# Kernel tuning notes

Measured on AMD Instinct MI355X. Metric: run time of the kernel, lower is better.

## Reference

```python
import jax, jax.numpy as jnp
import numpy as np

B = 16
C = 80
LEVELS = [(128, 128, 8), (64, 64, 16), (32, 32, 32), (16, 16, 64), (8, 8, 128)]
TOPN = 1000
MIN_SCORE = 0.05
NMS_THR = 0.6
MAX_OBJ = 100


def setup_inputs() -> dict:
    key = jax.random.key(0)
    inp = {}
    for l, (H, W, s) in enumerate(LEVELS):
        key, k1, k2, k3 = jax.random.split(key, 4)
        inp[f"cls{l}"] = jax.random.uniform(k1, (B, H, W, C), jnp.float32)
        inp[f"reg{l}"] = jax.random.uniform(k2, (B, H, W, 4), jnp.float32) * 128.0
        inp[f"ctr{l}"] = jax.random.uniform(k3, (B, H, W, 1), jnp.float32)
        xs = (jnp.arange(W, dtype=jnp.float32) + 0.5) * s
        ys = (jnp.arange(H, dtype=jnp.float32) + 0.5) * s
        gx, gy = jnp.meshgrid(xs, ys)  # [H, W]
        pos = jnp.stack([gx, gy], axis=-1)  # [H, W, 2]
        inp[f"pos{l}"] = jnp.broadcast_to(pos, (B, H, W, 2))
    return inp


def _nms_one(scores, classes, bboxes):
    # scores [N], classes int32 [N], bboxes float [N, 4] (already int-truncated values)
    s = jnp.where(scores > MIN_SCORE, scores, -jnp.inf)  # score-threshold mask
    top_s, top_i = jax.lax.top_k(s, TOPN)  # sort descending, keep topn
    top_c = jax.lax.stop_gradient(classes[top_i].astype(jnp.float32))
    top_b = bboxes[top_i]
    valid = top_s > MIN_SCORE
    wh = top_b[:, 2:4] - top_b[:, 0:2]
    areas = jnp.clip(wh[:, 0] * wh[:, 1], 0.0001)
    ar = jnp.arange(TOPN)

    def body(i, suppressed):
        active = valid[i] & (~suppressed[i])
        b = top_b[i]
        tl = jnp.maximum(b[0:2], top_b[:, 0:2])
        br = jnp.minimum(b[2:4], top_b[:, 2:4])
        owh = jnp.clip(br - tl, 0.0)
        inter = owh[:, 0] * owh[:, 1]
        union = jnp.clip(areas[i] + areas - inter, 0.0001)
        iou = inter / union
        return suppressed | (active & (ar > i) & (iou >= NMS_THR))

    suppressed = jax.lax.fori_loop(0, TOPN, body, jnp.zeros((TOPN,), bool))
    keep = valid & (~suppressed)
    rank = jnp.cumsum(keep.astype(jnp.int32)) - 1
    # scatter kept detections (in score order) into first MAX_OBJ slots; slot MAX_OBJ is a dump
    idx = jnp.where(keep & (rank < MAX_OBJ), rank, MAX_OBJ)
    out_s = jnp.full((MAX_OBJ + 1,), -1.0, jnp.float32).at[idx].set(jnp.where(keep, top_s, -1.0))[:MAX_OBJ]
    out_c = jnp.full((MAX_OBJ + 1,), -1.0, jnp.float32).at[idx].set(jnp.where(keep, top_c, -1.0))[:MAX_OBJ]
    out_b = jnp.zeros((MAX_OBJ + 1, 4), jnp.float32).at[idx].set(jnp.where(keep[:, None], top_b, 0.0))[:MAX_OBJ]
    return out_s, out_c, out_b


def _forward(cls_list, reg_list, ctr_list, pos_list):
    ss, cc, bb = [], [], []
    for c, r, t, p in zip(cls_list, reg_list, ctr_list, pos_list):
        b = c.shape[0]
        c = c.reshape(b, -1, c.shape[-1])   # [B, HW, 80]
        r = r.reshape(b, -1, 4)             # [B, HW, 4]
        t = t.reshape(b, -1)                # [B, HW]
        p = p.reshape(b, -1, 2)             # [B, HW, 2]
        sc = jnp.sqrt(jnp.max(c, axis=2) * t)
        cl = jnp.argmax(c, axis=2).astype(jnp.int32)
        bmin = p - r[:, :, 0:2]
        bmax = p + r[:, :, 2:4]
        # torch .int() truncates toward zero; values are used as floats afterward
        box = jax.lax.stop_gradient(jnp.trunc(jnp.concatenate([bmin, bmax], axis=2)))
        ss.append(sc); cc.append(cl); bb.append(box)
    scores = jnp.concatenate(ss, axis=1)
    classes = jnp.concatenate(cc, axis=1)
    boxes = jnp.concatenate(bb, axis=1)
    return jax.vmap(_nms_one)(scores, classes, boxes)


def reference(cls0, cls1, cls2, cls3, cls4, reg0, reg1, reg2, reg3, reg4,
              ctr0, ctr1, ctr2, ctr3, ctr4, pos0, pos1, pos2, pos3, pos4):
    return _forward([cls0, cls1, cls2, cls3, cls4],
                    [reg0, reg1, reg2, reg3, reg4],
                    [ctr0, ctr1, ctr2, ctr3, ctr4],
                    [pos0, pos1, pos2, pos3, pos4])
```

## Files before the change

kernel.cpp:

```cpp
#include <hip/hip_runtime.h>
#include <stdint.h>

typedef unsigned int u32;
typedef unsigned long long u64;

#define NTOT 21824
#define NBATCH 16
#define TOPN 1000
#define MAXOBJ 100
#define CAPC 8192
#define BINBASE 15616
#define NBINS 1024

__device__ __forceinline__ void locate(
    int b, int loc,
    const float* __restrict__ cls0, const float* __restrict__ cls1,
    const float* __restrict__ cls2, const float* __restrict__ cls3,
    const float* __restrict__ cls4,
    const float* __restrict__ ctr0, const float* __restrict__ ctr1,
    const float* __restrict__ ctr2, const float* __restrict__ ctr3,
    const float* __restrict__ ctr4,
    const float*& cp, const float*& tp)
{
    if (loc < 16384)      { size_t o = (size_t)b*16384 + loc;          cp = cls0 + o*80; tp = ctr0 + o; }
    else if (loc < 20480) { size_t o = (size_t)b*4096  + (loc-16384);  cp = cls1 + o*80; tp = ctr1 + o; }
    else if (loc < 21504) { size_t o = (size_t)b*1024  + (loc-20480);  cp = cls2 + o*80; tp = ctr2 + o; }
    else if (loc < 21760) { size_t o = (size_t)b*256   + (loc-21504);  cp = cls3 + o*80; tp = ctr3 + o; }
    else                  { size_t o = (size_t)b*64    + (loc-21760);  cp = cls4 + o*80; tp = ctr4 + o; }
}

__global__ __launch_bounds__(256) void decode_kernel(
    const float* __restrict__ cls0, const float* __restrict__ cls1,
    const float* __restrict__ cls2, const float* __restrict__ cls3,
    const float* __restrict__ cls4,
    const float* __restrict__ ctr0, const float* __restrict__ ctr1,
    const float* __restrict__ ctr2, const float* __restrict__ ctr3,
    const float* __restrict__ ctr4,
    u32* __restrict__ keys, int* __restrict__ clsidx)
{
    int tid = threadIdx.x;
    int g = tid >> 2, j = tid & 3;
    int b = blockIdx.y;
    int loc0 = blockIdx.x * 128 + g;
    int loc1 = loc0 + 64;
    bool v1 = (loc1 < NTOT);

    const float *cp0, *tp0, *cp1, *tp1;
    locate(b, loc0, cls0, cls1, cls2, cls3, cls4, ctr0, ctr1, ctr2, ctr3, ctr4, cp0, tp0);
    locate(b, v1 ? loc1 : loc0, cls0, cls1, cls2, cls3, cls4, ctr0, ctr1, ctr2, ctr3, ctr4, cp1, tp1);

    const float4* c40 = (const float4*)cp0;
    const float4* c41 = (const float4*)cp1;
    float4 a0[5], a1[5];
#pragma unroll
    for (int q = 0; q < 5; ++q) a0[q] = c40[j + 4*q];
#pragma unroll
    for (int q = 0; q < 5; ++q) a1[q] = c41[j + 4*q];
    float t0v = *tp0;
    float t1v = *tp1;

    float maxv0 = -1.0f; int arg0 = 0;
    float maxv1 = -1.0f; int arg1 = 0;
#pragma unroll
    for (int q = 0; q < 5; ++q) {
        float4 v = a0[q];
        int ch = 16*q + 4*j;
        if (v.x > maxv0) { maxv0 = v.x; arg0 = ch;     }
        if (v.y > maxv0) { maxv0 = v.y; arg0 = ch + 1; }
        if (v.z > maxv0) { maxv0 = v.z; arg0 = ch + 2; }
        if (v.w > maxv0) { maxv0 = v.w; arg0 = ch + 3; }
    }
#pragma unroll
    for (int q = 0; q < 5; ++q) {
        float4 v = a1[q];
        int ch = 16*q + 4*j;
        if (v.x > maxv1) { maxv1 = v.x; arg1 = ch;     }
        if (v.y > maxv1) { maxv1 = v.y; arg1 = ch + 1; }
        if (v.z > maxv1) { maxv1 = v.z; arg1 = ch + 2; }
        if (v.w > maxv1) { maxv1 = v.w; arg1 = ch + 3; }
    }
#pragma unroll
    for (int d = 1; d <= 2; d <<= 1) {
        float ov = __shfl_xor(maxv0, d);
        int   oa = __shfl_xor(arg0, d);
        if (ov > maxv0 || (ov == maxv0 && oa < arg0)) { maxv0 = ov; arg0 = oa; }
        float ow = __shfl_xor(maxv1, d);
        int   ob = __shfl_xor(arg1, d);
        if (ow > maxv1 || (ow == maxv1 && ob < arg1)) { maxv1 = ow; arg1 = ob; }
    }
    if (j == 0) {
        float score0 = sqrtf(maxv0 * t0v);
        u32 key0 = (score0 > 0.05f) ? (__float_as_uint(score0) | 0x80000000u) : 0u;
        size_t o0 = (size_t)b * NTOT + loc0;
        keys[o0] = key0;
        clsidx[o0] = arg0;
        if (v1) {
            float score1 = sqrtf(maxv1 * t1v);
            u32 key1 = (score1 > 0.05f) ? (__float_as_uint(score1) | 0x80000000u) : 0u;
            size_t o1 = (size_t)b * NTOT + loc1;
            keys[o1] = key1;
            clsidx[o1] = arg1;
        }
    }
}

__global__ __launch_bounds__(1024) void pivot_kernel(
    const u32* __restrict__ keys, u32* __restrict__ params, u32* __restrict__ gcnt,
    float* __restrict__ tscore, float* __restrict__ tcls, float4* __restrict__ tbox)
{
    __shared__ u32 shist[NBINS];
    __shared__ u32 s_wtot[16];
    __shared__ int s_tf;
    int b = blockIdx.x, tid = threadIdx.x;
    int lane = tid & 63, wave = tid >> 6;
    const u32* kb = keys + (size_t)b * NTOT;

    for (int i = tid; i < TOPN; i += 1024) {
        size_t o = (size_t)b * TOPN + i;
        tscore[o] = -1.0f; tcls[o] = -1.0f;
        tbox[o] = make_float4(0.f, 0.f, 0.f, 0.f);
    }
    shist[tid] = 0;
    if (tid == 0) { s_tf = -1; gcnt[b * 32] = 0; }
    __syncthreads();

    for (int i = tid; i < NTOT; i += 1024) {
        u32 k = kb[i];
        if (k) {
            int v = (int)((k >> 16) & 0x7FFFu) - BINBASE;
            v = v < 0 ? 0 : (v > NBINS - 1 ? NBINS - 1 : v);
            atomicAdd(&shist[v], 1u);
        }
    }
    __syncthreads();

    u32 h = shist[tid];
    u32 x = h;
#pragma unroll
    for (int off = 1; off < 64; off <<= 1) {
        u32 y = __shfl_down(x, off);
        if (lane + off < 64) x += y;
    }
    if (lane == 0) s_wtot[wave] = x;
    __syncthreads();
    u32 wsuf = 0, tot = 0;
    for (int w2 = 0; w2 < 16; ++w2) { u32 v = s_wtot[w2]; tot += v; if (w2 > wave) wsuf += v; }
    u32 suffix_incl = x + wsuf;
    u32 target = (tot < TOPN) ? tot : TOPN;

    if (target > 0 && suffix_incl >= target) atomicMax(&s_tf, tid);
    __syncthreads();
    if (tid == 0) {
        int t0 = s_tf;
        u32 P;
        if (target == 0)        P = 0xFFFFFFFFu;
        else if (tot <= TOPN)   P = 1u;
        else                    P = ((u32)(t0 + BINBASE) << 16) | 0x80000000u;
        params[2 * b] = P;
        params[2 * b + 1] = target;
    }
}

__global__ __launch_bounds__(256) void gather_kernel(
    const u32* __restrict__ keys, const u32* __restrict__ params,
    u64* __restrict__ candbuf, u32* __restrict__ gcnt)
{
    __shared__ u32 s_wcnt[4];
    __shared__ u32 s_base;
    int b = blockIdx.y;
    int tid = threadIdx.x;
    int lane = tid & 63, wave = tid >> 6;
    u32 P = params[2 * b];
    int i = blockIdx.x * 256 + tid;
    u32 k = (i < NTOT) ? keys[(size_t)b * NTOT + i] : 0u;
    bool pass = (k != 0u) && (k >= P);
    u64 mask = __ballot(pass);
    if (lane == 0) s_wcnt[wave] = (u32)__popcll(mask);
    __syncthreads();
    if (tid == 0) {
        u32 tot = s_wcnt[0] + s_wcnt[1] + s_wcnt[2] + s_wcnt[3];
        s_base = tot ? atomicAdd(&gcnt[b * 32], tot) : 0u;
    }
    __syncthreads();
    if (pass) {
        u32 woff = 0;
        for (int w2 = 0; w2 < wave; ++w2) woff += s_wcnt[w2];
        u32 pos = s_base + woff + (u32)__popcll(mask & ((1ull << lane) - 1ull));
        if (pos < CAPC)
            candbuf[(size_t)b * CAPC + pos] = ((u64)k << 32) | (u32)(~i);
    }
}

__global__ __launch_bounds__(256) void rank_kernel(
    const u64* __restrict__ candbuf, const u32* __restrict__ gcnt,
    const u32* __restrict__ params,
    const int* __restrict__ clsidx,
    const float* __restrict__ reg0, const float* __restrict__ reg1,
    const float* __restrict__ reg2, const float* __restrict__ reg3,
    const float* __restrict__ reg4,
    float* __restrict__ tscore, float* __restrict__ tcls, float4* __restrict__ tbox)
{
    int b = blockIdx.y;
    int lane = threadIdx.x & 63;
    u32 M = gcnt[b * 32]; if (M > CAPC) M = CAPC;
    u32 target = params[2 * b + 1];
    const u64* cb = candbuf + (size_t)b * CAPC;
    u32 Mr = (M + 63u) & ~63u;

    u32 wbase0 = blockIdx.x * 256 + (threadIdx.x & ~63u);
    for (u32 base = wbase0; base < M; base += 8 * 256) {
        u32 i0 = base + lane;
        bool val = (i0 < M);
        u64 e = val ? cb[i0] : ~0ull;
        u32 r = 0;
        for (u32 c0 = 0; c0 < Mr; c0 += 64) {
            u32 j = c0 + lane;
            u64 v = (j < M) ? cb[j] : 0ull;
            u32 vlo = (u32)v, vhi = (u32)(v >> 32);
#pragma unroll
            for (int s = 0; s < 64; ++s) {
                u32 lo = (u32)__builtin_amdgcn_readlane((int)vlo, s);
                u32 hi = (u32)__builtin_amdgcn_readlane((int)vhi, s);
                u64 vj = ((u64)hi << 32) | lo;
                r += (vj > e) ? 1u : 0u;
            }
        }
        if (val && r < target) {
            u32 k = (u32)(e >> 32);
            u32 loc = ~(u32)e;
            const float* rp; float st; u32 li; int wsh;
            if (loc < 16384u)      { li = loc;          wsh = 7; st = 8.f;   rp = reg0 + ((size_t)b*16384 + li)*4; }
            else if (loc < 20480u) { li = loc - 16384u; wsh = 6; st = 16.f;  rp = reg1 + ((size_t)b*4096  + li)*4; }
            else if (loc < 21504u) { li = loc - 20480u; wsh = 5; st = 32.f;  rp = reg2 + ((size_t)b*1024  + li)*4; }
            else if (loc < 21760u) { li = loc - 21504u; wsh = 4; st = 64.f;  rp = reg3 + ((size_t)b*256   + li)*4; }
            else                   { li = loc - 21760u; wsh = 3; st = 128.f; rp = reg4 + ((size_t)b*64    + li)*4; }
            u32 wx = li & ((1u << wsh) - 1u);
            u32 hy = li >> wsh;
            float px = ((float)wx + 0.5f) * st;
            float py = ((float)hy + 0.5f) * st;
            float4 rg = *(const float4*)rp;
            float4 bx;
            bx.x = truncf(px - rg.x); bx.y = truncf(py - rg.y);
            bx.z = truncf(px + rg.z); bx.w = truncf(py + rg.w);
            size_t src = (size_t)b * NTOT + loc;
            size_t o = (size_t)b * TOPN + r;
            tscore[o] = __uint_as_float(k & 0x7FFFFFFFu);
            tcls[o] = (float)clsidx[src];
            tbox[o] = bx;
        }
    }
}

__global__ __launch_bounds__(256) void iou_kernel(
    const float4* __restrict__ tbox, u64* __restrict__ sup)
{
    __shared__ float4 sbox[TOPN];
    int b = blockIdx.y;
    int tid = threadIdx.x, lane = tid & 63, wave = tid >> 6;
    const float4* tb = tbox + (size_t)b * TOPN;
    for (int i = tid; i < TOPN; i += 256) sbox[i] = tb[i];
    __syncthreads();
    int i = blockIdx.x * 4 + wave;
    float4 bi = sbox[i];
    float areai = fmaxf((bi.z - bi.x) * (bi.w - bi.y), 0.0001f);
    u64* row = sup + ((size_t)b * TOPN + i) * 16;
#pragma unroll
    for (int w = 0; w < 16; ++w) {
        int col = w * 64 + lane;
        bool bit = false;
        if (col < TOPN) {
            float4 bj = sbox[col];
            float areaj = fmaxf((bj.z - bj.x) * (bj.w - bj.y), 0.0001f);
            float tlx = fmaxf(bi.x, bj.x), tly = fmaxf(bi.y, bj.y);
            float brx = fminf(bi.z, bj.z), bry = fminf(bi.w, bj.w);
            float ow = fmaxf(brx - tlx, 0.f), oh = fmaxf(bry - tly, 0.f);
            float inter = ow * oh;
            float uni = fmaxf(areai + areaj - inter, 0.0001f);
            bit = (col > i) && (inter / uni >= 0.6f);
        }
        u64 m = __ballot(bit);
        if (lane == 0) row[w] = m;
    }
}

#define CHROWS 128
#define NCHUNK 8

__global__ __launch_bounds__(1024) void finalize_kernel(
    const float* __restrict__ tscore, const float* __restrict__ tcls,
    const float4* __restrict__ tbox, const u64* __restrict__ sup,
    float* __restrict__ out)
{
    __shared__ u64 mat[2][CHROWS * 16];
    __shared__ u32 validsh[TOPN];
    __shared__ u64 removed_sh[16];
    __shared__ u32 wpref[17];
    int b = blockIdx.x, tid = threadIdx.x;
    int wave = tid >> 6, lane = tid & 63;

    for (int i = tid; i < TOPN; i += 1024)
        validsh[i] = (tscore[(size_t)b * TOPN + i] > 0.05f) ? 1u : 0u;

    const u64* supb = sup + (size_t)b * TOPN * 16;
    for (int idx = tid; idx < CHROWS * 16; idx += 1024)
        mat[0][idx] = supb[idx];
    __syncthreads();

    u64 my = 0;
    if (wave == 0) {
#pragma unroll
        for (int w2 = 0; w2 < 16; ++w2) {
            int i = w2 * 64 + lane;
            bool v = (i < TOPN) ? (validsh[i] != 0) : false;
            u64 m = __ballot(v);
            if (lane == w2) my = ~m;
        }
    }

    for (int chunk = 0; chunk < NCHUNK; ++chunk) {
        if (wave > 0 && chunk + 1 < NCHUNK) {
            int nr = (chunk + 1 == NCHUNK - 1) ? (TOPN - (NCHUNK - 1) * CHROWS) : CHROWS;
            const u64* src = supb + (size_t)(chunk + 1) * CHROWS * 16;
            u64* dst = mat[(chunk + 1) & 1];
            for (int idx = tid - 64; idx < nr * 16; idx += 960)
                dst[idx] = src[idx];
        }
        if (wave == 0) {
            int r0 = chunk * CHROWS;
            int rows = (chunk == NCHUNK - 1) ? (TOPN - r0) : CHROWS;
            int lw = lane & 15;
            const u64* M = mat[chunk & 1];
            for (int sub = 0; sub < rows; sub += 64) {
                int w2 = (r0 + sub) >> 6;
                u64 cur = __shfl(my, w2);
                int nsub = rows - sub; if (nsub > 64) nsub = 64;
                const u64* R = M + sub * 16;
                int ngrp = nsub >> 3;
                u64 cme[8], cww[8];
#pragma unroll
                for (int g = 0; g < 8; ++g) { cme[g] = R[g*16 + lw]; cww[g] = R[g*16 + w2]; }
                for (int grp = 0; grp < ngrp; ++grp) {
                    u64 nme[8] = {0,0,0,0,0,0,0,0}, nww[8] = {0,0,0,0,0,0,0,0};
                    if (grp + 1 < ngrp) {
                        const u64* Rn = R + (grp + 1) * 128;
#pragma unroll
                        for (int g = 0; g < 8; ++g) { nme[g] = Rn[g*16 + lw]; nww[g] = Rn[g*16 + w2]; }
                    }
#pragma unroll
                    for (int g = 0; g < 8; ++g) {
                        int u = grp * 8 + g;
                        u64 bit = (cur >> u) & 1ull;
                        u64 act = bit - 1ull;
                        cur |= cww[g] & act;
                        my  |= cme[g] & act;
                    }
#pragma unroll
                    for (int g = 0; g < 8; ++g) { cme[g] = nme[g]; cww[g] = nww[g]; }
                }
            }
        }
        __syncthreads();
    }
    if (wave == 0) {
        if (lane < 16) removed_sh[lane] = my;
        u32 pc = (lane < 16) ? (u32)__popcll(~my) : 0u;
#pragma unroll
        for (int off = 1; off < 16; off <<= 1) {
            u32 y = __shfl_up(pc, off);
            if (lane >= off) pc += y;
        }
        if (lane < 16) wpref[lane + 1] = pc;
        if (lane == 0) wpref[0] = 0;
    }
    __syncthreads();

    float* out_s = out;
    float* out_c = out + NBATCH * MAXOBJ;
    float* out_b = out + 2 * NBATCH * MAXOBJ;
    if (tid < MAXOBJ)     { out_s[b * MAXOBJ + tid] = -1.f; out_c[b * MAXOBJ + tid] = -1.f; }
    if (tid < MAXOBJ * 4) out_b[b * MAXOBJ * 4 + tid] = 0.f;
    __syncthreads();
    if (tid < TOPN) {
        u64 kw = ~removed_sh[tid >> 6];
        if ((kw >> (tid & 63)) & 1ull) {
            int rank = (int)wpref[tid >> 6] + (int)__popcll(kw & ((1ull << (tid & 63)) - 1ull));
            if (rank < MAXOBJ) {
                size_t o = (size_t)b * TOPN + tid;
                out_s[b * MAXOBJ + rank] = tscore[o];
                out_c[b * MAXOBJ + rank] = tcls[o];
                ((float4*)out_b)[b * MAXOBJ + rank] = tbox[o];
            }
        }
    }
}

extern "C" void kernel_launch(void* const* d_in, const int* in_sizes, int n_in,
                              void* d_out, int out_size, void* d_ws, size_t ws_size,
                              hipStream_t stream) {
    (void)in_sizes; (void)n_in; (void)out_size; (void)ws_size;
    const float* cls[5]; const float* reg[5]; const float* ctr[5];
    for (int l = 0; l < 5; ++l) {
        cls[l] = (const float*)d_in[4 * l + 0];
        reg[l] = (const float*)d_in[4 * l + 1];
        ctr[l] = (const float*)d_in[4 * l + 2];
    }
    char* w = (char*)d_ws;
    u32*    keys   = (u32*)(w + 0);
    int*    clsidx = (int*)(w + 1396736);
    float*  tscore = (float*)(w + 2793472);
    float*  tcls   = (float*)(w + 2857472);
    float4* tbox   = (float4*)(w + 2921472);
    u64*    sup    = (u64*)(w + 3177472);
    u64*    candbuf= (u64*)(w + 3177472);
    u32*    gcnt   = (u32*)(w + 5225472);
    u32*    params = (u32*)(w + 5227520);

    decode_kernel<<<dim3((NTOT + 127) / 128, NBATCH), 256, 0, stream>>>(
        cls[0], cls[1], cls[2], cls[3], cls[4],
        ctr[0], ctr[1], ctr[2], ctr[3], ctr[4],
        keys, clsidx);
    pivot_kernel<<<NBATCH, 1024, 0, stream>>>(keys, params, gcnt, tscore, tcls, tbox);
    gather_kernel<<<dim3((NTOT + 255) / 256, NBATCH), 256, 0, stream>>>(keys, params, candbuf, gcnt);
    rank_kernel<<<dim3(8, NBATCH), 256, 0, stream>>>(candbuf, gcnt, params, clsidx,
                                                     reg[0], reg[1], reg[2], reg[3], reg[4],
                                                     tscore, tcls, tbox);
    iou_kernel<<<dim3(TOPN / 4, NBATCH), 256, 0, stream>>>(tbox, sup);
    finalize_kernel<<<NBATCH, 1024, 0, stream>>>(tscore, tcls, tbox, sup, (float*)d_out);
}
```

Baseline: 269.6 us.

## Fuse pivot, gather and rank into one per-batch top-k kernel with LDS candidates

Merges the histogram-pivot, candidate-gather and rank kernels into a single 1024-thread block per batch image. Candidates are compacted into shared memory instead of a global buffer, and the rank pass reads them from LDS. This removes two launches and the global round trips for params, counters and candidates. The cost is that the O(M²) ranking now runs on only 16 blocks instead of 128, which cuts parallelism, and 64KB of LDS is used per block. Decode also handles four locations per thread instead of two.

```diff
diff --git a/kernel.cpp b/kernel.cpp
--- a/kernel.cpp
+++ b/kernel.cpp
@@ -8,7 +8,7 @@
 #define NBATCH 16
 #define TOPN 1000
 #define MAXOBJ 100
-#define CAPC 8192
+#define LCAP 8192
 #define BINBASE 15616
 #define NBINS 1024
 
@@ -41,76 +41,77 @@
     int tid = threadIdx.x;
     int g = tid >> 2, j = tid & 3;
     int b = blockIdx.y;
-    int loc0 = blockIdx.x * 128 + g;
-    int loc1 = loc0 + 64;
-    bool v1 = (loc1 < NTOT);
-
-    const float *cp0, *tp0, *cp1, *tp1;
-    locate(b, loc0, cls0, cls1, cls2, cls3, cls4, ctr0, ctr1, ctr2, ctr3, ctr4, cp0, tp0);
-    locate(b, v1 ? loc1 : loc0, cls0, cls1, cls2, cls3, cls4, ctr0, ctr1, ctr2, ctr3, ctr4, cp1, tp1);
-
-    const float4* c40 = (const float4*)cp0;
-    const float4* c41 = (const float4*)cp1;
-    float4 a0[5], a1[5];
-#pragma unroll
-    for (int q = 0; q < 5; ++q) a0[q] = c40[j + 4*q];
-#pragma unroll
-    for (int q = 0; q < 5; ++q) a1[q] = c41[j + 4*q];
-    float t0v = *tp0;
-    float t1v = *tp1;
-
-    float maxv0 = -1.0f; int arg0 = 0;
-    float maxv1 = -1.0f; int arg1 = 0;
-#pragma unroll
-    for (int q = 0; q < 5; ++q) {
-        float4 v = a0[q];
-        int ch = 16*q + 4*j;
-        if (v.x > maxv0) { maxv0 = v.x; arg0 = ch;     }
-        if (v.y > maxv0) { maxv0 = v.y; arg0 = ch + 1; }
-        if (v.z > maxv0) { maxv0 = v.z; arg0 = ch + 2; }
-        if (v.w > maxv0) { maxv0 = v.w; arg0 = ch + 3; }
-    }
-#pragma unroll
-    for (int q = 0; q < 5; ++q) {
-        float4 v = a1[q];
-        int ch = 16*q + 4*j;
-        if (v.x > maxv1) { maxv1 = v.x; arg1 = ch;     }
-        if (v.y > maxv1) { maxv1 = v.y; arg1 = ch + 1; }
-        if (v.z > maxv1) { maxv1 = v.z; arg1 = ch + 2; }
-        if (v.w > maxv1) { maxv1 = v.w; arg1 = ch + 3; }
+    int base = blockIdx.x * 256;
+
+    const float* cp[4]; const float* tp[4]; bool v[4];
+#pragma unroll
+    for (int c = 0; c < 4; ++c) {
+        v[c] = (base + 64 * c) < NTOT;
+        int loc = v[c] ? (base + 64 * c + g) : (base + g);
+        locate(b, loc, cls0, cls1, cls2, cls3, cls4,
+               ctr0, ctr1, ctr2, ctr3, ctr4, cp[c], tp[c]);
+    }
+
+    float4 a[4][5];
+#pragma unroll
+    for (int c = 0; c < 4; ++c) {
+        const float4* c4 = (const float4*)cp[c];
+#pragma unroll
+        for (int q = 0; q < 5; ++q) a[c][q] = c4[j + 4*q];
+    }
+    float tv[4];
+#pragma unroll
+    for (int c = 0; c < 4; ++c) tv[c] = *tp[c];
+
+    float maxv[4]; int arg[4];
+#pragma unroll
+    for (int c = 0; c < 4; ++c) {
+        maxv[c] = -1.0f; arg[c] = 0;
+#pragma unroll
+        for (int q = 0; q < 5; ++q) {
+            float4 vv = a[c][q];
+            int ch = 16*q + 4*j;
+            if (vv.x > maxv[c]) { maxv[c] = vv.x; arg[c] = ch;     }
+            if (vv.y > maxv[c]) { maxv[c] = vv.y; arg[c] = ch + 1; }
+            if (vv.z > maxv[c]) { maxv[c] = vv.z; arg[c] = ch + 2; }
+            if (vv.w > maxv[c]) { maxv[c] = vv.w; arg[c] = ch + 3; }
+        }
     }
 #pragma unroll
     for (int d = 1; d <= 2; d <<= 1) {
-        float ov = __shfl_xor(maxv0, d);
-        int   oa = __shfl_xor(arg0, d);
-        if (ov > maxv0 || (ov == maxv0 && oa < arg0)) { maxv0 = ov; arg0 = oa; }
-        float ow = __shfl_xor(maxv1, d);
-        int   ob = __shfl_xor(arg1, d);
-        if (ow > maxv1 || (ow == maxv1 && ob < arg1)) { maxv1 = ow; arg1 = ob; }
+#pragma unroll
+        for (int c = 0; c < 4; ++c) {
+            float ov = __shfl_xor(maxv[c], d);
+            int   oa = __shfl_xor(arg[c], d);
+            if (ov > maxv[c] || (ov == maxv[c] && oa < arg[c])) { maxv[c] = ov; arg[c] = oa; }
+        }
     }
     if (j == 0) {
-        float score0 = sqrtf(maxv0 * t0v);
-        u32 key0 = (score0 > 0.05f) ? (__float_as_uint(score0) | 0x80000000u) : 0u;
-        size_t o0 = (size_t)b * NTOT + loc0;
-        keys[o0] = key0;
-        clsidx[o0] = arg0;
-        if (v1) {
-            float score1 = sqrtf(maxv1 * t1v);
-            u32 key1 = (score1 > 0.05f) ? (__float_as_uint(score1) | 0x80000000u) : 0u;
-            size_t o1 = (size_t)b * NTOT + loc1;
-            keys[o1] = key1;
-            clsidx[o1] = arg1;
-        }
-    }
-}
-
-__global__ __launch_bounds__(1024) void pivot_kernel(
-    const u32* __restrict__ keys, u32* __restrict__ params, u32* __restrict__ gcnt,
+#pragma unroll
+        for (int c = 0; c < 4; ++c) {
+            if (v[c]) {
+                float score = sqrtf(maxv[c] * tv[c]);
+                u32 key = (score > 0.05f) ? (__float_as_uint(score) | 0x80000000u) : 0u;
+                size_t o = (size_t)b * NTOT + base + 64 * c + g;
+                keys[o] = key;
+                clsidx[o] = arg[c];
+            }
+        }
+    }
+}
+
+__global__ __launch_bounds__(1024) void topk_kernel(
+    const u32* __restrict__ keys, const int* __restrict__ clsidx,
+    const float* __restrict__ reg0, const float* __restrict__ reg1,
+    const float* __restrict__ reg2, const float* __restrict__ reg3,
+    const float* __restrict__ reg4,
     float* __restrict__ tscore, float* __restrict__ tcls, float4* __restrict__ tbox)
 {
+    __shared__ u64 cand[LCAP];
     __shared__ u32 shist[NBINS];
     __shared__ u32 s_wtot[16];
     __shared__ int s_tf;
+    __shared__ u32 s_cnt;
     int b = blockIdx.x, tid = threadIdx.x;
     int lane = tid & 63, wave = tid >> 6;
     const u32* kb = keys + (size_t)b * NTOT;
@@ -121,7 +122,7 @@
         tbox[o] = make_float4(0.f, 0.f, 0.f, 0.f);
     }
     shist[tid] = 0;
-    if (tid == 0) { s_tf = -1; gcnt[b * 32] = 0; }
+    if (tid == 0) { s_tf = -1; s_cnt = 0; }
     __syncthreads();
 
     for (int i = tid; i < NTOT; i += 1024) {
@@ -150,73 +151,40 @@
 
     if (target > 0 && suffix_incl >= target) atomicMax(&s_tf, tid);
     __syncthreads();
-    if (tid == 0) {
+    u32 P;
+    {
         int t0 = s_tf;
-        u32 P;
         if (target == 0)        P = 0xFFFFFFFFu;
         else if (tot <= TOPN)   P = 1u;
         else                    P = ((u32)(t0 + BINBASE) << 16) | 0x80000000u;
-        params[2 * b] = P;
-        params[2 * b + 1] = target;
-    }
-}
-
-__global__ __launch_bounds__(256) void gather_kernel(
-    const u32* __restrict__ keys, const u32* __restrict__ params,
-    u64* __restrict__ candbuf, u32* __restrict__ gcnt)
-{
-    __shared__ u32 s_wcnt[4];
-    __shared__ u32 s_base;
-    int b = blockIdx.y;
-    int tid = threadIdx.x;
-    int lane = tid & 63, wave = tid >> 6;
-    u32 P = params[2 * b];
-    int i = blockIdx.x * 256 + tid;
-    u32 k = (i < NTOT) ? keys[(size_t)b * NTOT + i] : 0u;
-    bool pass = (k != 0u) && (k >= P);
-    u64 mask = __ballot(pass);
-    if (lane == 0) s_wcnt[wave] = (u32)__popcll(mask);
-    __syncthreads();
-    if (tid == 0) {
-        u32 tot = s_wcnt[0] + s_wcnt[1] + s_wcnt[2] + s_wcnt[3];
-        s_base = tot ? atomicAdd(&gcnt[b * 32], tot) : 0u;
-    }
-    __syncthreads();
-    if (pass) {
-        u32 woff = 0;
-        for (int w2 = 0; w2 < wave; ++w2) woff += s_wcnt[w2];
-        u32 pos = s_base + woff + (u32)__popcll(mask & ((1ull << lane) - 1ull));
-        if (pos < CAPC)
-            candbuf[(size_t)b * CAPC + pos] = ((u64)k << 32) | (u32)(~i);
-    }
-}
-
-__global__ __launch_bounds__(256) void rank_kernel(
-    const u64* __restrict__ candbuf, const u32* __restrict__ gcnt,
-    const u32* __restrict__ params,
-    const int* __restrict__ clsidx,
-    const float* __restrict__ reg0, const float* __restrict__ reg1,
-    const float* __restrict__ reg2, const float* __restrict__ reg3,
-    const float* __restrict__ reg4,
-    float* __restrict__ tscore, float* __restrict__ tcls, float4* __restrict__ tbox)
-{
-    int b = blockIdx.y;
-    int lane = threadIdx.x & 63;
-    u32 M = gcnt[b * 32]; if (M > CAPC) M = CAPC;
-    u32 target = params[2 * b + 1];
-    const u64* cb = candbuf + (size_t)b * CAPC;
+    }
+
+    for (int base = 0; base < NTOT; base += 1024) {
+        int i = base + tid;
+        u32 k = (i < NTOT) ? kb[i] : 0u;
+        bool pass = (k != 0u) && (k >= P);
+        u64 mask = __ballot(pass);
+        u32 wbase = 0;
+        if (lane == 0 && mask) wbase = atomicAdd(&s_cnt, (u32)__popcll(mask));
+        wbase = __shfl(wbase, 0);
+        if (pass) {
+            u32 pos = wbase + (u32)__popcll(mask & ((1ull << lane) - 1ull));
+            if (pos < LCAP) cand[pos] = ((u64)k << 32) | (u32)(~i);
+        }
+    }
+    __syncthreads();
+    u32 M = s_cnt; if (M > LCAP) M = LCAP;
     u32 Mr = (M + 63u) & ~63u;
 
-    u32 wbase0 = blockIdx.x * 256 + (threadIdx.x & ~63u);
-    for (u32 base = wbase0; base < M; base += 8 * 256) {
+    for (u32 base = wave * 64; base < M; base += 16 * 64) {
         u32 i0 = base + lane;
         bool val = (i0 < M);
-        u64 e = val ? cb[i0] : ~0ull;
+        u64 e = val ? cand[i0] : ~0ull;
         u32 r = 0;
         for (u32 c0 = 0; c0 < Mr; c0 += 64) {
-            u32 j = c0 + lane;
-            u64 v = (j < M) ? cb[j] : 0ull;
-            u32 vlo = (u32)v, vhi = (u32)(v >> 32);
+            u32 jj = c0 + lane;
+            u64 vv = (jj < M) ? cand[jj] : 0ull;
+            u32 vlo = (u32)vv, vhi = (u32)(vv >> 32);
 #pragma unroll
             for (int s = 0; s < 64; ++s) {
                 u32 lo = (u32)__builtin_amdgcn_readlane((int)vlo, s);
@@ -411,19 +379,14 @@
     float*  tcls   = (float*)(w + 2857472);
     float4* tbox   = (float4*)(w + 2921472);
     u64*    sup    = (u64*)(w + 3177472);
-    u64*    candbuf= (u64*)(w + 3177472);
-    u32*    gcnt   = (u32*)(w + 5225472);
-    u32*    params = (u32*)(w + 5227520);
-
-    decode_kernel<<<dim3((NTOT + 127) / 128, NBATCH), 256, 0, stream>>>(
+
+    decode_kernel<<<dim3((NTOT + 255) / 256, NBATCH), 256, 0, stream>>>(
         cls[0], cls[1], cls[2], cls[3], cls[4],
         ctr[0], ctr[1], ctr[2], ctr[3], ctr[4],
         keys, clsidx);
-    pivot_kernel<<<NBATCH, 1024, 0, stream>>>(keys, params, gcnt, tscore, tcls, tbox);
-    gather_kernel<<<dim3((NTOT + 255) / 256, NBATCH), 256, 0, stream>>>(keys, params, candbuf, gcnt);
-    rank_kernel<<<dim3(8, NBATCH), 256, 0, stream>>>(candbuf, gcnt, params, clsidx,
-                                                     reg[0], reg[1], reg[2], reg[3], reg[4],
-                                                     tscore, tcls, tbox);
+    topk_kernel<<<NBATCH, 1024, 0, stream>>>(keys, clsidx,
+                                             reg[0], reg[1], reg[2], reg[3], reg[4],
+                                             tscore, tcls, tbox);
     iou_kernel<<<dim3(TOPN / 4, NBATCH), 256, 0, stream>>>(tbox, sup);
     finalize_kernel<<<NBATCH, 1024, 0, stream>>>(tscore, tcls, tbox, sup, (float*)d_out);
 }
```

Measured after the change: 299.4 us. +11.0%, slower.
